# Kernel optimization log

Hardware: AMD Instinct MI355X
Metric: run time of the kernel (lower is better)

Reference implementation:

```python
import jax, jax.numpy as jnp
import numpy as np

# dims
D_IN, D, H, HD = 1536, 256, 8, 32
DEPTH, FFN = 2, 1024
B, L = 1, 8191
NGRIDS, TILE = 256, 256
SEGMENTS = [1024, 2048, 4096, 8192, 16384]   # get_optimal_segment_length(32768, 256)
RATIOS = [1, 2, 4, 8, 16]                    # LongNet canonical dilation ratios
SCALE = HD ** -0.5


def setup_inputs() -> dict:
    key = jax.random.key(0)
    ks = jax.random.split(key, 16)
    w = lambda k, s: jax.random.normal(k, s, jnp.float32) * 0.02
    return {
        "x": jax.random.normal(ks[0], (B, L, D_IN), jnp.float32),
        "coords": jax.random.randint(ks[1], (B, L, 2), 0, NGRIDS * TILE, jnp.int32),
        "proj_w": w(ks[2], (D_IN, D)), "proj_b": jnp.zeros((D,), jnp.float32),
        "cls_tok": w(ks[3], (1, 1, D)),
        "Wq": w(ks[4], (DEPTH, D, D)), "Wk": w(ks[5], (DEPTH, D, D)),
        "Wv": w(ks[6], (DEPTH, D, D)), "Wo": w(ks[7], (DEPTH, D, D)),
        "bq": jnp.zeros((DEPTH, D), jnp.float32), "bk": jnp.zeros((DEPTH, D), jnp.float32),
        "bv": jnp.zeros((DEPTH, D), jnp.float32), "bo": jnp.zeros((DEPTH, D), jnp.float32),
        "ln1_g": jnp.ones((DEPTH, D), jnp.float32), "ln1_b": jnp.zeros((DEPTH, D), jnp.float32),
        "ln2_g": jnp.ones((DEPTH, D), jnp.float32), "ln2_b": jnp.zeros((DEPTH, D), jnp.float32),
        "W1": w(ks[8], (DEPTH, D, FFN)), "b1": jnp.zeros((DEPTH, FFN), jnp.float32),
        "W2": w(ks[9], (DEPTH, FFN, D)), "b2": jnp.zeros((DEPTH, D), jnp.float32),
        "enc_g": jnp.ones((D,), jnp.float32), "enc_b": jnp.zeros((D,), jnp.float32),
        "norm_g": jnp.ones((D,), jnp.float32), "norm_b": jnp.zeros((D,), jnp.float32),
    }


def _ln(x, g, b):
    mu = x.mean(-1, keepdims=True)
    v = ((x - mu) ** 2).mean(-1, keepdims=True)
    return (x - mu) * jax.lax.rsqrt(v + 1e-5) * g + b


def _pos_table():
    # MAE-style 2D sincos pos embed, row 0 = cls (zeros). [NGRIDS^2+1, D]
    g = jnp.arange(NGRIDS, dtype=jnp.float32)
    gw, gh = jnp.meshgrid(g, g)  # gw[i,j]=j, gh[i,j]=i; flatten index = i*NGRIDS + j
    def one(pos):
        omega = 1.0 / (10000.0 ** (jnp.arange(D // 4, dtype=jnp.float32) / (D // 4)))
        o = pos.reshape(-1)[:, None] * omega[None]
        return jnp.concatenate([jnp.sin(o), jnp.cos(o)], -1)
    tab = jnp.concatenate([one(gw), one(gh)], -1)
    return jnp.concatenate([jnp.zeros((1, D), jnp.float32), tab], 0)


def _dilated_attn(q, k, v):
    # q,k,v: [B,S,H,HD]. LongNet: per (segment w, dilation r) branch, sparse in-segment
    # attention on stride-r rows (head-dependent offset h%r), branches fused via their
    # softmax log-sum-exp weights.
    S = q.shape[1]
    hh = jnp.arange(H)[:, None]
    outs, lses = [], []
    for w, r in zip(SEGMENTS, RATIOS):
        n = (S + w - 1) // w
        Sp = n * w
        def seg(t):
            tp = jnp.pad(t, ((0, 0), (0, Sp - S), (0, 0), (0, 0)))
            return tp.reshape(B, n, w, H, HD).transpose(0, 1, 3, 2, 4)  # [B,n,H,w,HD]
        qs_, ks_, vs_ = seg(q), seg(k), seg(v)
        t = w // r
        idx = (hh % r) + r * jnp.arange(t)[None, :]                  # [H,t]
        qs = qs_[:, :, hh, idx]                                      # [B,n,H,t,HD]
        ks = ks_[:, :, hh, idx]
        vs = vs_[:, :, hh, idx]
        valid = (jnp.arange(n)[:, None, None] * w + idx[None]) < S   # [n,H,t]
        sc = jnp.einsum('bnhtd,bnhsd->bnhts', qs, ks) * SCALE
        sc = jnp.where(valid[None, :, :, None, :], sc, -1e9)
        m = sc.max(-1, keepdims=True)
        p = jnp.exp(sc - m)
        den = p.sum(-1, keepdims=True)
        o = jnp.einsum('bnhts,bnhsd->bnhtd', p, vs) / den
        lse = m[..., 0] + jnp.log(den[..., 0])                       # [B,n,H,t]
        fo = jnp.zeros((B, n, H, w, HD), q.dtype).at[:, :, hh, idx].set(o)
        fl = jnp.full((B, n, H, w), -1e30, q.dtype).at[:, :, hh, idx].set(lse)
        outs.append(fo.transpose(0, 1, 3, 2, 4).reshape(B, Sp, H, HD)[:, :S])
        lses.append(fl.transpose(0, 1, 3, 2).reshape(B, Sp, H)[:, :S])
    Ls = jnp.stack(lses)   # [5,B,S,H]
    Os = jnp.stack(outs)   # [5,B,S,H,HD]
    wts = jnp.exp(Ls - Ls.max(0, keepdims=True))
    return (wts[..., None] * Os).sum(0) / wts.sum(0)[..., None]


def _forward(x, coords, proj_w, proj_b, cls_tok, Wq, Wk, Wv, Wo, bq, bk, bv, bo,
             ln1_g, ln1_b, ln2_g, ln2_b, W1, b1, W2, b2, enc_g, enc_b, norm_g, norm_b):
    h = x @ proj_w + proj_b                                   # patch embed [B,L,D]
    tab = _pos_table()
    cg = jnp.floor(coords.astype(jnp.float32) / TILE).astype(jnp.int32)
    pos = cg[..., 0] * NGRIDS + cg[..., 1] + 1                # coords_to_pos
    h = h + tab[pos]
    cls = jnp.broadcast_to(cls_tok + tab[0], (B, 1, D))
    h = jnp.concatenate([cls, h], 1)                          # [B,S,D], S = L+1
    S = h.shape[1]
    for i in range(DEPTH):                                    # pre-LN LongNet encoder layers
        a = _ln(h, ln1_g[i], ln1_b[i])
        q = (a @ Wq[i] + bq[i]).reshape(B, S, H, HD)
        k = (a @ Wk[i] + bk[i]).reshape(B, S, H, HD)
        v = (a @ Wv[i] + bv[i]).reshape(B, S, H, HD)
        o = _dilated_attn(q, k, v).reshape(B, S, D)
        h = h + o @ Wo[i] + bo[i]
        f = _ln(h, ln2_g[i], ln2_b[i])
        h = h + jax.nn.gelu(f @ W1[i] + b1[i], approximate=False) @ W2[i] + b2[i]
    h = _ln(h, enc_g, enc_b)     # encoder final LN
    h = _ln(h, norm_g, norm_b)   # model self.norm
    return h[:, 0]               # cls embedding (global_pool=False)


def reference(x, coords, proj_w, proj_b, cls_tok, Wq, Wk, Wv, Wo, bq, bk, bv, bo,
              ln1_g, ln1_b, ln2_g, ln2_b, W1, b1, W2, b2, enc_g, enc_b, norm_g, norm_b):
    return _forward(x, coords, proj_w, proj_b, cls_tok, Wq, Wk, Wv, Wo, bq, bk, bv, bo,
                    ln1_g, ln1_b, ln2_g, ln2_b, W1, b1, W2, b2, enc_g, enc_b, norm_g, norm_b)
```

## Files before the change

kernel.cpp:

```cpp
#include <hip/hip_runtime.h>
#include <math.h>

#define S_TOT 8192
#define DD 256
#define NHEAD 8
#define HDSZ 32
#define ATT_SCALE 0.17677669529663687f
#define ATT_SCALE_LOG2E 0.25506601f

typedef short short8 __attribute__((ext_vector_type(8)));
typedef short short4v __attribute__((ext_vector_type(4)));
typedef float f32x4 __attribute__((ext_vector_type(4)));
typedef unsigned short ushort;

#define OFF_PROJ 0
#define OFF_WQ0  393216
#define OFF_WK0  458752
#define OFF_WV0  524288
#define OFF_WO0  589824
#define OFF_W10  655360
#define OFF_W20  917504
#define OFF_WK1  1179648
#define OFF_WV1  1245184
#define OFF_WQ1  1310720
#define OFF_WO1  1376256
#define OFF_W11  1441792
#define OFF_W21  1703936
#define WBUF_TOT 1966080

__device__ inline ushort f2bf(float f) {
    union { float f; unsigned u; } c; c.f = f;
    unsigned u = c.u;
    u += 0x7fffu + ((u >> 16) & 1u);
    return (ushort)(u >> 16);
}
__device__ inline float bf2f(ushort u) {
    union { unsigned u; float f; } c; c.u = ((unsigned)u) << 16;
    return c.f;
}
__device__ inline float gelu_exact(float v) {
    return 0.5f * v * (1.0f + erff(v * 0.7071067811865475f));
}
__device__ inline unsigned cvtpk_bf16(float a, float b) {
    unsigned r;
    asm("v_cvt_pk_bf16_f32 %0, %1, %2" : "=v"(r) : "v"(a), "v"(b));
    return r;
}
__device__ inline short8 cat44(short4v a, short4v b) {
    return __builtin_shufflevector(a, b, 0, 1, 2, 3, 4, 5, 6, 7);
}
__device__ inline float block_sum256(float v, float* red) {
    #pragma unroll
    for (int off = 32; off > 0; off >>= 1) v += __shfl_down(v, off, 64);
    const int wid = threadIdx.x >> 6, lane = threadIdx.x & 63;
    if (lane == 0) red[wid] = v;
    __syncthreads();
    const float s = red[0] + red[1] + red[2] + red[3];
    __syncthreads();
    return s;
}

__global__ __launch_bounds__(256)
void setup_kernel(const float* __restrict__ x, const float* __restrict__ proj_w,
                  const float* __restrict__ Wq, const float* __restrict__ Wk,
                  const float* __restrict__ Wv, const float* __restrict__ Wo,
                  const float* __restrict__ W1, const float* __restrict__ W2,
                  const float* __restrict__ bq, const float* __restrict__ bk,
                  const float* __restrict__ bv, const float* __restrict__ cls_tok,
                  ushort* __restrict__ wbuf, float* __restrict__ bqkv0,
                  float* __restrict__ bkv1, ushort* __restrict__ xbf,
                  float* __restrict__ h)
{
    const int b = blockIdx.x;
    const int t = threadIdx.x;
    if (b >= 482) {
        if (b == 6626) { h[t] = cls_tok[t]; return; }
        const int i = (b - 482) * 256 + t;
        const int n8 = 8191 * 1536 / 8;
        if (i >= n8) return;
        const float4 a0 = *(const float4*)(x + (size_t)i * 8);
        const float4 a1 = *(const float4*)(x + (size_t)i * 8 + 4);
        ushort tmp[8] = { f2bf(a0.x), f2bf(a0.y), f2bf(a0.z), f2bf(a0.w),
                          f2bf(a1.x), f2bf(a1.y), f2bf(a1.z), f2bf(a1.w) };
        *(uint4*)(xbf + (size_t)i * 8) = *(const uint4*)tmp;
        return;
    }
    if (b >= 480) {
        if (b == 480) {
            for (int i = t; i < 768; i += 256)
                bqkv0[i] = (i < 256) ? bq[i] : ((i < 512) ? bk[i - 256] : bv[i - 512]);
        } else {
            for (int i = t; i < 512; i += 256)
                bkv1[i] = (i < 256) ? bk[256 + i] : bv[i];
        }
        return;
    }
    const float* src; ushort* dst; int R, C, t0;
    if (b < 96)       { src = proj_w;        dst = wbuf + OFF_PROJ; R = 1536; C = 256;  t0 = 0;   }
    else if (b < 112) { src = Wq;            dst = wbuf + OFF_WQ0;  R = 256;  C = 256;  t0 = 96;  }
    else if (b < 128) { src = Wk;            dst = wbuf + OFF_WK0;  R = 256;  C = 256;  t0 = 112; }
    else if (b < 144) { src = Wv;            dst = wbuf + OFF_WV0;  R = 256;  C = 256;  t0 = 128; }
    else if (b < 160) { src = Wo;            dst = wbuf + OFF_WO0;  R = 256;  C = 256;  t0 = 144; }
    else if (b < 224) { src = W1;            dst = wbuf + OFF_W10;  R = 256;  C = 1024; t0 = 160; }
    else if (b < 288) { src = W2;            dst = wbuf + OFF_W20;  R = 1024; C = 256;  t0 = 224; }
    else if (b < 304) { src = Wk + 65536;    dst = wbuf + OFF_WK1;  R = 256;  C = 256;  t0 = 288; }
    else if (b < 320) { src = Wv + 65536;    dst = wbuf + OFF_WV1;  R = 256;  C = 256;  t0 = 304; }
    else if (b < 336) { src = Wq + 65536;    dst = wbuf + OFF_WQ1;  R = 256;  C = 256;  t0 = 320; }
    else if (b < 352) { src = Wo + 65536;    dst = wbuf + OFF_WO1;  R = 256;  C = 256;  t0 = 336; }
    else if (b < 416) { src = W1 + 262144;   dst = wbuf + OFF_W11;  R = 256;  C = 1024; t0 = 352; }
    else              { src = W2 + 262144;   dst = wbuf + OFF_W21;  R = 1024; C = 256;  t0 = 416; }
    const int lt = b - t0;
    const int tC = C >> 6;
    const int tr = lt / tC, tc = lt % tC;
    __shared__ ushort tile[64][68];
    const int col = t & 63;
    const int r4  = t >> 6;
    #pragma unroll
    for (int i = 0; i < 16; ++i) {
        const int row = i * 4 + r4;
        tile[row][col] = f2bf(src[(size_t)(tr * 64 + row) * C + tc * 64 + col]);
    }
    __syncthreads();
    #pragma unroll
    for (int i = 0; i < 16; ++i) {
        const int n = i * 4 + r4;
        dst[(size_t)(tc * 64 + n) * R + tr * 64 + col] = tile[col][n];
    }
}

__global__ __launch_bounds__(256)
void ln_kernel(const float* __restrict__ in, const float* __restrict__ g,
               const float* __restrict__ b, ushort* __restrict__ outp)
{
    const int row  = blockIdx.x * 4 + (threadIdx.x >> 6);
    const int lane = threadIdx.x & 63;
    const float4 xv = *(const float4*)(in + (size_t)row * DD + lane * 4);
    float s = (xv.x + xv.y) + (xv.z + xv.w);
    #pragma unroll
    for (int off = 32; off > 0; off >>= 1) s += __shfl_xor(s, off, 64);
    const float mu = s * (1.0f / 256.0f);
    const float dx = xv.x - mu, dy = xv.y - mu, dz = xv.z - mu, dw = xv.w - mu;
    float v2 = (dx * dx + dy * dy) + (dz * dz + dw * dw);
    #pragma unroll
    for (int off = 32; off > 0; off >>= 1) v2 += __shfl_xor(v2, off, 64);
    const float rs = rsqrtf(v2 * (1.0f / 256.0f) + 1e-5f);
    const float4 gv = *(const float4*)(g + lane * 4);
    const float4 bv = *(const float4*)(b + lane * 4);
    uint2 w;
    w.x = cvtpk_bf16(dx * rs * gv.x + bv.x, dy * rs * gv.y + bv.y);
    w.y = cvtpk_bf16(dz * rs * gv.z + bv.z, dw * rs * gv.w + bv.w);
    *(uint2*)(outp + (size_t)row * DD + lane * 4) = w;
}

template <int BN>
__global__ __launch_bounds__(256)
void gemm4_kernel(const ushort* __restrict__ A, const ushort* __restrict__ Bt,
                  const float* __restrict__ bias, void* __restrict__ Cv,
                  int M, int N, int K, int flags, const int* __restrict__ coords)
{
    __shared__ ushort As[3][64][64];
    __shared__ ushort Bs[3][BN][64];
    constexpr int NT = BN / 32;
    const int nx  = N / BN;
    const int ny8 = gridDim.x / (8 * nx);
    const int b   = blockIdx.x;
    const int c8  = b & 7;
    const int j   = b >> 3;
    const int m0  = (c8 * ny8 + j / nx) * 64;
    const int n0  = (j % nx) * BN;

    const int tid  = threadIdx.x;
    const int wave = tid >> 6;
    const int lane = tid & 63;
    const int lrow = lane & 15;
    const int quad = lane >> 4;
    const int wr = (wave >> 1) * 32;
    const int wc = (wave & 1) * (BN / 2);

    float* Cf  = (float*)Cv;
    ushort* Cb = (ushort*)Cv;

    f32x4 acc[2][NT];
    #pragma unroll
    for (int mt = 0; mt < 2; ++mt)
        #pragma unroll
        for (int nt = 0; nt < NT; ++nt)
            acc[mt][nt] = (f32x4){0.f, 0.f, 0.f, 0.f};

    const int srow = tid >> 3;
    const int scol = (tid & 7) * 16;

    #define STAGE(BUF, KK)                                                        \
    do {                                                                          \
        _Pragma("unroll")                                                         \
        for (int c = 0; c < 2; ++c) {                                             \
            const int row = c * 32 + srow;                                        \
            const int sb  = scol ^ ((row & 7) << 4);                              \
            const ushort* srcp = A + (size_t)(m0 + row) * K + (KK) + (sb >> 1);   \
            __builtin_amdgcn_global_load_lds(                                     \
                (const __attribute__((address_space(1))) void*)srcp,              \
                (__attribute__((address_space(3))) void*)&As[BUF][c * 32 + wave * 8][0], \
                16, 0, 0);                                                        \
        }                                                                         \
        _Pragma("unroll")                                                         \
        for (int c = 0; c < BN / 32; ++c) {                                       \
            const int row = c * 32 + srow;                                        \
            const int sb  = scol ^ ((row & 7) << 4);                              \
            const ushort* srcp = Bt + (size_t)(n0 + row) * K + (KK) + (sb >> 1);  \
            __builtin_amdgcn_global_load_lds(                                     \
                (const __attribute__((address_space(1))) void*)srcp,              \
                (__attribute__((address_space(3))) void*)&Bs[BUF][c * 32 + wave * 8][0], \
                16, 0, 0);                                                        \
        }                                                                         \
    } while (0)

    #define COMPUTE(BUF)                                                          \
    do {                                                                          \
        _Pragma("unroll")                                                         \
        for (int ks = 0; ks < 2; ++ks) {                                          \
            short8 af[2], bfr[NT];                                                \
            _Pragma("unroll")                                                     \
            for (int mt = 0; mt < 2; ++mt) {                                      \
                const int row = wr + mt * 16 + lrow;                              \
                const int cb  = (ks * 64 + quad * 16) ^ ((row & 7) << 4);         \
                af[mt] = *(const short8*)((const char*)&As[BUF][row][0] + cb);    \
            }                                                                     \
            _Pragma("unroll")                                                     \
            for (int nt = 0; nt < NT; ++nt) {                                     \
                const int row = wc + nt * 16 + lrow;                              \
                const int cb  = (ks * 64 + quad * 16) ^ ((row & 7) << 4);         \
                bfr[nt] = *(const short8*)((const char*)&Bs[BUF][row][0] + cb);   \
            }                                                                     \
            _Pragma("unroll")                                                     \
            for (int mt = 0; mt < 2; ++mt)                                        \
                _Pragma("unroll")                                                 \
                for (int nt = 0; nt < NT; ++nt)                                   \
                    acc[mt][nt] = __builtin_amdgcn_mfma_f32_16x16x32_bf16(        \
                                      af[mt], bfr[nt], acc[mt][nt], 0, 0, 0);     \
        }                                                                         \
    } while (0)

    #define WAIT_BAR(NVM)                                                         \
    do {                                                                          \
        asm volatile("s_waitcnt vmcnt(" #NVM ")" ::: "memory");                   \
        __builtin_amdgcn_sched_barrier(0);                                        \
        __builtin_amdgcn_s_barrier();                                             \
        __builtin_amdgcn_sched_barrier(0);                                        \
    } while (0)

    const int ktiles = K >> 6;
    STAGE(0, 0);
    STAGE(1, 64);
    int bt = 0;
    for (int t = 0; t < ktiles - 2; ++t) {
        WAIT_BAR(4);
        const int nb = (bt + 2 >= 3) ? bt - 1 : bt + 2;
        STAGE(nb, (t + 2) * 64);
        COMPUTE(bt);
        bt = (bt + 1 == 3) ? 0 : bt + 1;
    }
    WAIT_BAR(4);
    COMPUTE(bt);
    bt = (bt + 1 == 3) ? 0 : bt + 1;
    WAIT_BAR(0);
    COMPUTE(bt);
    #undef STAGE
    #undef COMPUTE
    #undef WAIT_BAR

    #pragma unroll
    for (int mt = 0; mt < 2; ++mt) {
        #pragma unroll
        for (int rg = 0; rg < 4; ++rg) {
            const int r = m0 + wr + mt * 16 + quad * 4 + rg;
            if (r >= M) continue;
            #pragma unroll
            for (int nt = 0; nt < NT; ++nt) {
                const int c = n0 + wc + nt * 16 + lrow;
                float vv = acc[mt][nt][rg] + bias[c];
                if (flags & 8) {
                    const int cg = coords[2 * r + ((c < 128) ? 1 : 0)] >> 8;
                    const float omega = exp2f((float)(c & 63) * -0.2076205059304703f);
                    const float o = (float)cg * omega;
                    vv += ((c & 64) == 0) ? __sinf(o) : __cosf(o);
                }
                if (flags & 16) { if (c < 256) vv *= ATT_SCALE_LOG2E; }
                if (flags & 2) vv = gelu_exact(vv);
                if (flags & 4) {
                    Cb[(size_t)r * N + c] = f2bf(vv);
                } else {
                    if (flags & 1) vv += Cf[(size_t)r * N + c];
                    Cf[(size_t)r * N + c] = vv;
                }
            }
        }
    }
}

__global__ __launch_bounds__(256)
void attn_mfma_kernel(const ushort* __restrict__ q, const ushort* __restrict__ k,
                      const ushort* __restrict__ v, float* __restrict__ bo5,
                      float* __restrict__ lse5, int qs)
{
    __shared__ ushort Kb[2][64][40];
    __shared__ ushort Vt[2][32][72];

    const int unit = blockIdx.x;
    const int segu = unit >> 3;
    const int head = unit & 7;
    int b2, n;
    if (segu < 8)        { b2 = 0; n = segu; }
    else if (segu < 12)  { b2 = 1; n = segu - 8; }
    else if (segu < 14)  { b2 = 2; n = segu - 12; }
    else if (segu == 14) { b2 = 3; n = 0; }
    else                 { b2 = 4; n = 0; }
    const int w  = 1024 << b2;
    const int rr = 1 << b2;
    const int base = n * w + (head & (rr - 1));

    int kEnd = (S_TOT - base + rr - 1) >> b2;
    if (kEnd > 1024) kEnd = 1024;
    if (blockIdx.y * 128 >= kEnd) return;

    const int tid  = threadIdx.x;
    const int wave = tid >> 6;
    const int lane = tid & 63;
    const int lrow = lane & 15;
    const int quad = lane >> 4;

    short8 qf[2];
    #pragma unroll
    for (int m = 0; m < 2; ++m) {
        const int j  = blockIdx.y * 128 + wave * 32 + m * 16 + lrow;
        const int pq = base + rr * j;
        qf[m] = *(const short8*)(q + (size_t)pq * qs + head * HDSZ + quad * 8);
    }

    const short8 ones8 = {0x3F80, 0x3F80, 0x3F80, 0x3F80,
                          0x3F80, 0x3F80, 0x3F80, 0x3F80};

    f32x4 acc[2][2];
    f32x4 acc_l[2];
    #pragma unroll
    for (int m = 0; m < 2; ++m) {
        #pragma unroll
        for (int dt = 0; dt < 2; ++dt) acc[m][dt] = (f32x4){0.f, 0.f, 0.f, 0.f};
        acc_l[m] = (f32x4){0.f, 0.f, 0.f, 0.f};
    }

    const int skr = tid >> 2;
    const int sdb = (tid & 3) * 8;
    const int grp = tid & 3;
    const int wcol = (2 * skr + 32 * grp) & 127;

    size_t prow = (size_t)(base + rr * skr) * qs + head * HDSZ + sdb;
    uint4 kreg = *(const uint4*)(k + prow);
    uint4 vreg = *(const uint4*)(v + prow);

    *(uint4*)&Kb[0][skr][sdb] = kreg;
    {
        const ushort* vp = (const ushort*)&vreg;
        #pragma unroll
        for (int i = 0; i < 8; ++i)
            *(ushort*)((char*)&Vt[0][sdb + i][0] + wcol) = vp[i];
    }

    int cur = 0;
    for (int kc = 0; kc < kEnd; kc += 64) {
        __syncthreads();
        const bool more = (kc + 64 < kEnd);
        if (more) {
            prow = (size_t)(base + rr * (kc + 64 + skr)) * qs + head * HDSZ + sdb;
            kreg = *(const uint4*)(k + prow);
            vreg = *(const uint4*)(v + prow);
        }

        short8 kf[4];
        #pragma unroll
        for (int t = 0; t < 4; ++t)
            kf[t] = *(const short8*)&Kb[cur][t * 16 + lrow][quad * 8];

        short8 vf[2][2];
        #pragma unroll
        for (int g = 0; g < 2; ++g)
            #pragma unroll
            for (int dt = 0; dt < 2; ++dt) {
                const int row  = dt * 16 + lrow;
                const int rotb = 32 * ((row >> 3) & 3);
                const int cb0  = (64 * g + 8 * quad + rotb) & 127;
                const int cb1  = (64 * g + 8 * quad + 32 + rotb) & 127;
                vf[g][dt] = cat44(*(const short4v*)((const char*)&Vt[cur][row][0] + cb0),
                                  *(const short4v*)((const char*)&Vt[cur][row][0] + cb1));
            }

        #pragma unroll
        for (int m = 0; m < 2; ++m) {
            f32x4 sc[4];
            #pragma unroll
            for (int t = 0; t < 4; ++t)
                sc[t] = __builtin_amdgcn_mfma_f32_16x16x32_bf16(
                            kf[t], qf[m], (f32x4){0.f,0.f,0.f,0.f}, 0, 0, 0);
            float p[4][4];
            #pragma unroll
            for (int t = 0; t < 4; ++t)
                #pragma unroll
                for (int rg = 0; rg < 4; ++rg)
                    p[t][rg] = exp2f(sc[t][rg]);
            unsigned pw[4][2];
            #pragma unroll
            for (int t = 0; t < 4; ++t) {
                pw[t][0] = cvtpk_bf16(p[t][0], p[t][1]);
                pw[t][1] = cvtpk_bf16(p[t][2], p[t][3]);
            }
            #pragma unroll
            for (int g = 0; g < 2; ++g) {
                union { short8 s; unsigned u[4]; } pa;
                pa.u[0] = pw[2 * g][0];
                pa.u[1] = pw[2 * g][1];
                pa.u[2] = pw[2 * g + 1][0];
                pa.u[3] = pw[2 * g + 1][1];
                #pragma unroll
                for (int dt = 0; dt < 2; ++dt)
                    acc[m][dt] = __builtin_amdgcn_mfma_f32_16x16x32_bf16(
                                     pa.s, vf[g][dt], acc[m][dt], 0, 0, 0);
                acc_l[m] = __builtin_amdgcn_mfma_f32_16x16x32_bf16(
                               pa.s, ones8, acc_l[m], 0, 0, 0);
            }
        }

        if (more) {
            *(uint4*)&Kb[cur ^ 1][skr][sdb] = kreg;
            const ushort* vp = (const ushort*)&vreg;
            #pragma unroll
            for (int i = 0; i < 8; ++i)
                *(ushort*)((char*)&Vt[cur ^ 1][sdb + i][0] + wcol) = vp[i];
        }
        cur ^= 1;
    }

    #pragma unroll
    for (int m = 0; m < 2; ++m) {
        #pragma unroll
        for (int rg = 0; rg < 4; ++rg) {
            const float li = acc_l[m][rg];
            const int j  = blockIdx.y * 128 + wave * 32 + m * 16 + quad * 4 + rg;
            const int pq = base + rr * j;
            const float inv = 1.0f / li;
            float* dst = bo5 + ((size_t)b2 * S_TOT + pq) * DD + head * HDSZ;
            dst[lrow]      = acc[m][0][rg] * inv;
            dst[16 + lrow] = acc[m][1][rg] * inv;
            if (lrow == 0)
                lse5[((size_t)b2 * S_TOT + pq) * NHEAD + head] = __logf(li);
        }
    }
}

__global__ __launch_bounds__(64)
void attn_row0_kernel(const float* __restrict__ q, const ushort* __restrict__ k,
                      const ushort* __restrict__ v, float* __restrict__ bo5,
                      float* __restrict__ lse5, int kvs)
{
    const int b2 = blockIdx.x >> 3;
    const int head = blockIdx.x & 7;
    const int r = 1 << b2;
    if (head & (r - 1)) return;
    const int tid = threadIdx.x;
    float qreg[32];
    #pragma unroll
    for (int d = 0; d < 32; d += 4) {
        const float4 t4 = *(const float4*)(q + head * HDSZ + d);
        qreg[d] = t4.x; qreg[d+1] = t4.y; qreg[d+2] = t4.z; qreg[d+3] = t4.w;
    }
    float m = -3.0e38f, l = 0.f, o[32];
    #pragma unroll
    for (int d = 0; d < 32; ++d) o[d] = 0.f;
    for (int j = tid; j < 1024; j += 64) {
        const int pk = r * j;
        float s;
        if (pk < S_TOT) {
            float s0 = 0.f;
            #pragma unroll
            for (int d = 0; d < 32; d += 8) {
                const uint4 raw = *(const uint4*)(k + (size_t)pk * kvs + head * HDSZ + d);
                const ushort* kp = (const ushort*)&raw;
                #pragma unroll
                for (int i = 0; i < 8; ++i) s0 += qreg[d + i] * bf2f(kp[i]);
            }
            s = s0 * ATT_SCALE;
        } else s = -1.0e9f;
        const float mn = fmaxf(m, s);
        const float c = __expf(m - mn);
        const float e = __expf(s - mn);
        l = l * c + e; m = mn;
        if (pk < S_TOT) {
            #pragma unroll
            for (int d = 0; d < 32; d += 8) {
                const uint4 raw = *(const uint4*)(v + (size_t)pk * kvs + head * HDSZ + d);
                const ushort* vp = (const ushort*)&raw;
                #pragma unroll
                for (int i = 0; i < 8; ++i) o[d + i] = o[d + i] * c + e * bf2f(vp[i]);
            }
        } else {
            #pragma unroll
            for (int d = 0; d < 32; ++d) o[d] *= c;
        }
    }
    __shared__ float ms[64], ls[64], os[64][32];
    ms[tid] = m; ls[tid] = l;
    #pragma unroll
    for (int d = 0; d < 32; ++d) os[tid][d] = o[d];
    __syncthreads();
    for (int st = 32; st >= 1; st >>= 1) {
        if (tid < st) {
            const float m2 = ms[tid + st], l2 = ls[tid + st];
            const float mn = fmaxf(ms[tid], m2);
            const float c1 = __expf(ms[tid] - mn);
            const float c2 = __expf(m2 - mn);
            ls[tid] = ls[tid] * c1 + l2 * c2;
            ms[tid] = mn;
            for (int d = 0; d < 32; ++d) os[tid][d] = os[tid][d]*c1 + os[tid+st][d]*c2;
        }
        __syncthreads();
    }
    if (tid < 32) bo5[(size_t)b2 * S_TOT * DD + head * HDSZ + tid] = os[0][tid] / ls[0];
    if (tid == 0) lse5[(size_t)b2 * S_TOT * NHEAD + head] = ms[0] + __logf(ls[0]);
}

__global__ __launch_bounds__(256)
void combine_kernel(const float* __restrict__ bo5, const float* __restrict__ lse5,
                    ushort* __restrict__ attn)
{
    const int p = blockIdx.x;
    const int d = threadIdx.x;
    const int h = d >> 5;
    float lse[5];
    bool sel[5];
    float mx = -3.0e38f;
    #pragma unroll
    for (int b2 = 0; b2 < 5; ++b2) {
        const int r = 1 << b2;
        sel[b2] = ((p & (r - 1)) == (h & (r - 1)));
        if (sel[b2]) {
            lse[b2] = lse5[((size_t)b2 * S_TOT + p) * NHEAD + h];
            mx = fmaxf(mx, lse[b2]);
        }
    }
    float wsum = 0.f, acc = 0.f;
    #pragma unroll
    for (int b2 = 0; b2 < 5; ++b2) {
        if (sel[b2]) {
            const float wgt = __expf(lse[b2] - mx);
            wsum += wgt;
            acc += wgt * bo5[((size_t)b2 * S_TOT + p) * DD + d];
        }
    }
    attn[(size_t)p * DD + d] = f2bf(acc / wsum);
}

__global__ __launch_bounds__(256)
void tail_qrow_kernel(const float* __restrict__ h, const float* __restrict__ g,
                      const float* __restrict__ b, const ushort* __restrict__ Wt,
                      const float* __restrict__ bias, float* __restrict__ qrow0)
{
    __shared__ float red[4];
    __shared__ float as[256];
    const int d = threadIdx.x;
    const float xv = h[d];
    const float mu = block_sum256(xv, red) * (1.0f / 256.0f);
    const float dv = xv - mu;
    const float var = block_sum256(dv * dv, red) * (1.0f / 256.0f);
    as[d] = dv * rsqrtf(var + 1e-5f) * g[d] + b[d];
    __syncthreads();
    float acc = 0.f;
    for (int k2 = 0; k2 < 256; k2 += 8) {
        const short8 w8 = *(const short8*)&Wt[(size_t)d * 256 + k2];
        #pragma unroll
        for (int j = 0; j < 8; ++j) acc += as[k2 + j] * bf2f((ushort)w8[j]);
    }
    qrow0[d] = acc + bias[d];
}

__global__ __launch_bounds__(256)
void tail_mid_kernel(const float* __restrict__ bo5, const float* __restrict__ lse5,
                     float* __restrict__ h, const ushort* __restrict__ Wo1t,
                     const float* __restrict__ bo1, const float* __restrict__ g2,
                     const float* __restrict__ b2, float* __restrict__ f)
{
    __shared__ float red[4];
    __shared__ float att[256];
    const int d = threadIdx.x;
    const int hh = d >> 5;
    float lse[5]; bool sel[5]; float mx = -3.0e38f;
    #pragma unroll
    for (int bb = 0; bb < 5; ++bb) {
        const int r = 1 << bb;
        sel[bb] = ((hh & (r - 1)) == 0);
        if (sel[bb]) {
            lse[bb] = lse5[(size_t)bb * S_TOT * NHEAD + hh];
            mx = fmaxf(mx, lse[bb]);
        }
    }
    float wsum = 0.f, acc = 0.f;
    #pragma unroll
    for (int bb = 0; bb < 5; ++bb) {
        if (sel[bb]) {
            const float wgt = __expf(lse[bb] - mx);
            wsum += wgt;
            acc += wgt * bo5[(size_t)bb * S_TOT * DD + d];
        }
    }
    att[d] = acc / wsum;
    __syncthreads();
    float a2 = 0.f;
    for (int k2 = 0; k2 < 256; k2 += 8) {
        const short8 w8 = *(const short8*)&Wo1t[(size_t)d * 256 + k2];
        #pragma unroll
        for (int j = 0; j < 8; ++j) a2 += att[k2 + j] * bf2f((ushort)w8[j]);
    }
    const float hv = a2 + bo1[d] + h[d];
    h[d] = hv;
    const float mu = block_sum256(hv, red) * (1.0f / 256.0f);
    const float dv = hv - mu;
    const float var = block_sum256(dv * dv, red) * (1.0f / 256.0f);
    f[d] = dv * rsqrtf(var + 1e-5f) * g2[d] + b2[d];
}

__global__ __launch_bounds__(256)
void tail_ffn1_kernel(const float* __restrict__ f, const ushort* __restrict__ W11t,
                      const float* __restrict__ b11, float* __restrict__ midr0)
{
    __shared__ float fs[256];
    const int tid = threadIdx.x;
    fs[tid] = f[tid];
    __syncthreads();
    const int n = blockIdx.x * 256 + tid;
    float acc = 0.f;
    for (int k2 = 0; k2 < 256; k2 += 8) {
        const short8 w8 = *(const short8*)&W11t[(size_t)n * 256 + k2];
        #pragma unroll
        for (int j = 0; j < 8; ++j) acc += fs[k2 + j] * bf2f((ushort)w8[j]);
    }
    midr0[n] = gelu_exact(acc + b11[n]);
}

__global__ __launch_bounds__(256)
void tail_ffn2_kernel(const float* __restrict__ midr0, const ushort* __restrict__ W21t,
                      const float* __restrict__ b21, float* __restrict__ h)
{
    __shared__ float ms[1024];
    const int tid = threadIdx.x;
    for (int i = tid; i < 1024; i += 256) ms[i] = midr0[i];
    __syncthreads();
    const int n  = blockIdx.x * 64 + (tid >> 2);
    const int kq = (tid & 3) * 256;
    float acc = 0.f;
    for (int k2 = 0; k2 < 256; k2 += 8) {
        const short8 w8 = *(const short8*)&W21t[(size_t)n * 1024 + kq + k2];
        #pragma unroll
        for (int j = 0; j < 8; ++j) acc += ms[kq + k2 + j] * bf2f((ushort)w8[j]);
    }
    acc += __shfl_xor(acc, 1);
    acc += __shfl_xor(acc, 2);
    if ((tid & 3) == 0) h[n] = h[n] + acc + b21[n];
}

__global__ __launch_bounds__(256)
void tail_final_kernel(const float* __restrict__ h, const float* __restrict__ eg,
                       const float* __restrict__ eb, const float* __restrict__ ng,
                       const float* __restrict__ nb, float* __restrict__ out)
{
    __shared__ float red[4];
    const int d = threadIdx.x;
    float xv = h[d];
    {
        const float mu = block_sum256(xv, red) * (1.0f / 256.0f);
        const float dv = xv - mu;
        const float var = block_sum256(dv * dv, red) * (1.0f / 256.0f);
        xv = dv * rsqrtf(var + 1e-5f) * eg[d] + eb[d];
    }
    {
        const float mu = block_sum256(xv, red) * (1.0f / 256.0f);
        const float dv = xv - mu;
        const float var = block_sum256(dv * dv, red) * (1.0f / 256.0f);
        out[d] = dv * rsqrtf(var + 1e-5f) * ng[d] + nb[d];
    }
}

extern "C" void kernel_launch(void* const* d_in, const int* in_sizes, int n_in,
                              void* d_out, int out_size, void* d_ws, size_t ws_size,
                              hipStream_t stream)
{
    const float* x      = (const float*)d_in[0];
    const int*   coords = (const int*)  d_in[1];
    const float* proj_w = (const float*)d_in[2];
    const float* proj_b = (const float*)d_in[3];
    const float* cls_tok= (const float*)d_in[4];
    const float* Wq     = (const float*)d_in[5];
    const float* Wk     = (const float*)d_in[6];
    const float* Wv     = (const float*)d_in[7];
    const float* Wo     = (const float*)d_in[8];
    const float* bq     = (const float*)d_in[9];
    const float* bk     = (const float*)d_in[10];
    const float* bv     = (const float*)d_in[11];
    const float* bo_    = (const float*)d_in[12];
    const float* ln1_g  = (const float*)d_in[13];
    const float* ln1_b  = (const float*)d_in[14];
    const float* ln2_g  = (const float*)d_in[15];
    const float* ln2_b  = (const float*)d_in[16];
    const float* W1     = (const float*)d_in[17];
    const float* b1     = (const float*)d_in[18];
    const float* W2     = (const float*)d_in[19];
    const float* b2v    = (const float*)d_in[20];
    const float* enc_g  = (const float*)d_in[21];
    const float* enc_b  = (const float*)d_in[22];
    const float* norm_g = (const float*)d_in[23];
    const float* norm_b = (const float*)d_in[24];
    float* out = (float*)d_out;

    const size_t SD = (size_t)S_TOT * DD;
    float* ws   = (float*)d_ws;
    float* h    = ws;
    float* big  = h + SD;
    float* bo5  = big;
    ushort* xbf   = (ushort*)big;
    ushort* midbf = (ushort*)big;
    float* lse5 = big + 5 * SD;
    ushort* a_bf    = (ushort*)(lse5 + 5 * S_TOT * NHEAD);
    ushort* qkv_bf  = a_bf + SD;
    ushort* attn_bf = qkv_bf + 3 * SD;
    ushort* wbuf    = attn_bf + SD;
    float* bqkv0  = (float*)(wbuf + WBUF_TOT);
    float* bkv1   = bqkv0 + 768;
    float* qrow0  = bkv1 + 512;
    float* f_r0   = qrow0 + 256;
    float* midr0  = f_r0 + 256;

    auto gemm64 = [&](const ushort* A, const ushort* Bt, const float* bias, void* C,
                      int M, int N, int K, int flags) {
        gemm4_kernel<64><<<128 * (N / 64), 256, 0, stream>>>(A, Bt, bias, C, M, N, K,
                                                             flags, coords);
    };

    setup_kernel<<<6627, 256, 0, stream>>>(x, proj_w, Wq, Wk, Wv, Wo, W1, W2,
                                           bq, bk, bv, cls_tok, wbuf, bqkv0, bkv1,
                                           xbf, h);

    gemm64(xbf, wbuf + OFF_PROJ, proj_b, h + DD, 8191, 256, 1536, 8);

    ln_kernel<<<S_TOT / 4, 256, 0, stream>>>(h, ln1_g, ln1_b, a_bf);
    gemm64(a_bf, wbuf + OFF_WQ0, bqkv0, qkv_bf, 8192, 768, 256, 4 | 16);
    attn_mfma_kernel<<<dim3(128, 8), 256, 0, stream>>>(qkv_bf, qkv_bf + 256,
                                                       qkv_bf + 512, bo5, lse5, 768);
    combine_kernel<<<S_TOT, 256, 0, stream>>>(bo5, lse5, attn_bf);
    gemm64(attn_bf, wbuf + OFF_WO0, bo_, h, 8192, 256, 256, 1);
    ln_kernel<<<S_TOT / 4, 256, 0, stream>>>(h, ln2_g, ln2_b, a_bf);
    gemm64(a_bf, wbuf + OFF_W10, b1, midbf, 8192, 1024, 256, 4 | 2);
    gemm64(midbf, wbuf + OFF_W20, b2v, h, 8192, 256, 1024, 1);

    ln_kernel<<<S_TOT / 4, 256, 0, stream>>>(h, ln1_g + 256, ln1_b + 256, a_bf);
    gemm64(a_bf, wbuf + OFF_WK1, bkv1, qkv_bf, 8192, 512, 256, 4);
    tail_qrow_kernel<<<1, 256, 0, stream>>>(h, ln1_g + 256, ln1_b + 256,
                                            wbuf + OFF_WQ1, bq + 256, qrow0);
    attn_row0_kernel<<<40, 64, 0, stream>>>(qrow0, qkv_bf, qkv_bf + 256, bo5, lse5, 512);
    tail_mid_kernel<<<1, 256, 0, stream>>>(bo5, lse5, h, wbuf + OFF_WO1, bo_ + 256,
                                           ln2_g + 256, ln2_b + 256, f_r0);
    tail_ffn1_kernel<<<4, 256, 0, stream>>>(f_r0, wbuf + OFF_W11, b1 + 1024, midr0);
    tail_ffn2_kernel<<<4, 256, 0, stream>>>(midr0, wbuf + OFF_W21, b2v + 256, h);
    tail_final_kernel<<<1, 256, 0, stream>>>(h, enc_g, enc_b, norm_g, norm_b, out);
}
```

Measured before the change: 378.9 us.

## Use 128-wide GEMM tiles for wide outputs and compute softmax row sums with VALU

The wide-N GEMMs (QKV, FFN1, layer-1 KV projections) now run with a BN=128 tile variant. Its pipeline wait counts are adjusted for the extra loads each stage issues. This halves the grid size and increases A-tile reuse per block. Separately, the attention kernel no longer spends an extra MFMA against a ones vector to get the softmax denominator. It sums the fp32 probabilities per lane and reduces them with cross-lane shuffles at the end, which also avoids summing bf16-rounded values.

```diff
diff --git a/kernel.cpp b/kernel.cpp
--- a/kernel.cpp
+++ b/kernel.cpp
@@ -240,9 +240,18 @@
         }                                                                         \
     } while (0)
 
-    #define WAIT_BAR(NVM)                                                         \
+    #define WAIT_BAR_N()                                                          \
     do {                                                                          \
-        asm volatile("s_waitcnt vmcnt(" #NVM ")" ::: "memory");                   \
+        if constexpr (BN == 64) { asm volatile("s_waitcnt vmcnt(4)" ::: "memory"); } \
+        else                    { asm volatile("s_waitcnt vmcnt(6)" ::: "memory"); } \
+        __builtin_amdgcn_sched_barrier(0);                                        \
+        __builtin_amdgcn_s_barrier();                                             \
+        __builtin_amdgcn_sched_barrier(0);                                        \
+    } while (0)
+
+    #define WAIT_BAR_0()                                                          \
+    do {                                                                          \
+        asm volatile("s_waitcnt vmcnt(0)" ::: "memory");                          \
         __builtin_amdgcn_sched_barrier(0);                                        \
         __builtin_amdgcn_s_barrier();                                             \
         __builtin_amdgcn_sched_barrier(0);                                        \
@@ -253,20 +262,21 @@
     STAGE(1, 64);
     int bt = 0;
     for (int t = 0; t < ktiles - 2; ++t) {
-        WAIT_BAR(4);
+        WAIT_BAR_N();
         const int nb = (bt + 2 >= 3) ? bt - 1 : bt + 2;
         STAGE(nb, (t + 2) * 64);
         COMPUTE(bt);
         bt = (bt + 1 == 3) ? 0 : bt + 1;
     }
-    WAIT_BAR(4);
+    WAIT_BAR_N();
     COMPUTE(bt);
     bt = (bt + 1 == 3) ? 0 : bt + 1;
-    WAIT_BAR(0);
+    WAIT_BAR_0();
     COMPUTE(bt);
     #undef STAGE
     #undef COMPUTE
-    #undef WAIT_BAR
+    #undef WAIT_BAR_N
+    #undef WAIT_BAR_0
 
     #pragma unroll
     for (int mt = 0; mt < 2; ++mt) {
@@ -336,17 +346,12 @@
         qf[m] = *(const short8*)(q + (size_t)pq * qs + head * HDSZ + quad * 8);
     }
 
-    const short8 ones8 = {0x3F80, 0x3F80, 0x3F80, 0x3F80,
-                          0x3F80, 0x3F80, 0x3F80, 0x3F80};
-
     f32x4 acc[2][2];
-    f32x4 acc_l[2];
-    #pragma unroll
-    for (int m = 0; m < 2; ++m) {
+    float lsum[2] = {0.f, 0.f};
+    #pragma unroll
+    for (int m = 0; m < 2; ++m)
         #pragma unroll
         for (int dt = 0; dt < 2; ++dt) acc[m][dt] = (f32x4){0.f, 0.f, 0.f, 0.f};
-        acc_l[m] = (f32x4){0.f, 0.f, 0.f, 0.f};
-    }
 
     const int skr = tid >> 2;
     const int sdb = (tid & 3) * 8;
@@ -406,6 +411,11 @@
                 #pragma unroll
                 for (int rg = 0; rg < 4; ++rg)
                     p[t][rg] = exp2f(sc[t][rg]);
+            float ps = 0.f;
+            #pragma unroll
+            for (int t = 0; t < 4; ++t)
+                ps += (p[t][0] + p[t][1]) + (p[t][2] + p[t][3]);
+            lsum[m] += ps;
             unsigned pw[4][2];
             #pragma unroll
             for (int t = 0; t < 4; ++t) {
@@ -423,8 +433,6 @@
                 for (int dt = 0; dt < 2; ++dt)
                     acc[m][dt] = __builtin_amdgcn_mfma_f32_16x16x32_bf16(
                                      pa.s, vf[g][dt], acc[m][dt], 0, 0, 0);
-                acc_l[m] = __builtin_amdgcn_mfma_f32_16x16x32_bf16(
-                               pa.s, ones8, acc_l[m], 0, 0, 0);
             }
         }
 
@@ -440,9 +448,12 @@
 
     #pragma unroll
     for (int m = 0; m < 2; ++m) {
+        float tot = lsum[m];
+        tot += __shfl_xor(tot, 16, 64);
+        tot += __shfl_xor(tot, 32, 64);
         #pragma unroll
         for (int rg = 0; rg < 4; ++rg) {
-            const float li = acc_l[m][rg];
+            const float li = __shfl(tot, quad * 4 + rg, 16);
             const int j  = blockIdx.y * 128 + wave * 32 + m * 16 + quad * 4 + rg;
             const int pq = base + rr * j;
             const float inv = 1.0f / li;
@@ -740,6 +751,11 @@
         gemm4_kernel<64><<<128 * (N / 64), 256, 0, stream>>>(A, Bt, bias, C, M, N, K,
                                                              flags, coords);
     };
+    auto gemm128 = [&](const ushort* A, const ushort* Bt, const float* bias, void* C,
+                       int M, int N, int K, int flags) {
+        gemm4_kernel<128><<<128 * (N / 128), 256, 0, stream>>>(A, Bt, bias, C, M, N, K,
+                                                               flags, coords);
+    };
 
     setup_kernel<<<6627, 256, 0, stream>>>(x, proj_w, Wq, Wk, Wv, Wo, W1, W2,
                                            bq, bk, bv, cls_tok, wbuf, bqkv0, bkv1,
@@ -748,17 +764,17 @@
     gemm64(xbf, wbuf + OFF_PROJ, proj_b, h + DD, 8191, 256, 1536, 8);
 
     ln_kernel<<<S_TOT / 4, 256, 0, stream>>>(h, ln1_g, ln1_b, a_bf);
-    gemm64(a_bf, wbuf + OFF_WQ0, bqkv0, qkv_bf, 8192, 768, 256, 4 | 16);
+    gemm128(a_bf, wbuf + OFF_WQ0, bqkv0, qkv_bf, 8192, 768, 256, 4 | 16);
     attn_mfma_kernel<<<dim3(128, 8), 256, 0, stream>>>(qkv_bf, qkv_bf + 256,
                                                        qkv_bf + 512, bo5, lse5, 768);
     combine_kernel<<<S_TOT, 256, 0, stream>>>(bo5, lse5, attn_bf);
     gemm64(attn_bf, wbuf + OFF_WO0, bo_, h, 8192, 256, 256, 1);
     ln_kernel<<<S_TOT / 4, 256, 0, stream>>>(h, ln2_g, ln2_b, a_bf);
-    gemm64(a_bf, wbuf + OFF_W10, b1, midbf, 8192, 1024, 256, 4 | 2);
+    gemm128(a_bf, wbuf + OFF_W10, b1, midbf, 8192, 1024, 256, 4 | 2);
     gemm64(midbf, wbuf + OFF_W20, b2v, h, 8192, 256, 1024, 1);
 
     ln_kernel<<<S_TOT / 4, 256, 0, stream>>>(h, ln1_g + 256, ln1_b + 256, a_bf);
-    gemm64(a_bf, wbuf + OFF_WK1, bkv1, qkv_bf, 8192, 512, 256, 4);
+    gemm128(a_bf, wbuf + OFF_WK1, bkv1, qkv_bf, 8192, 512, 256, 4);
     tail_qrow_kernel<<<1, 256, 0, stream>>>(h, ln1_g + 256, ln1_b + 256,
                                             wbuf + OFF_WQ1, bq + 256, qrow0);
     attn_row0_kernel<<<40, 64, 0, stream>>>(qrow0, qkv_bf, qkv_bf + 256, bo5, lse5, 512);
```

Measured after the change: 375.8 us. About the same (-0.8%).
